# Kernel optimization log

Hardware: AMD Instinct MI355X
Metric: run time of the kernel (lower is better)

## Reference

```python
import jax, jax.numpy as jnp
import numpy as np

B, N, D = 16, 2048, 256  # batch (pairs*2), num_keypoints, descriptor_dim


def setup_inputs() -> dict:
    key = jax.random.key(0)
    k1, k2, k3, k4 = jax.random.split(key, 4)
    descriptors = jax.random.normal(k1, (B, N, D), dtype=jnp.float32)
    mask = jax.random.randint(k2, (B, N), 0, 2, dtype=jnp.int32)
    proj_w = jax.random.normal(k3, (D, D), dtype=jnp.float32) * 0.02
    proj_b = jnp.zeros((D,), dtype=jnp.float32)
    match_w = jax.random.normal(k4, (1, D), dtype=jnp.float32) * 0.02
    match_b = jnp.zeros((1,), dtype=jnp.float32)
    return {"descriptors": descriptors, "mask": mask, "proj_w": proj_w,
            "proj_b": proj_b, "match_w": match_w, "match_b": match_b}


def reference(descriptors, mask, proj_w, proj_b, match_w, match_b):
    batch, n, d = descriptors.shape
    pairs = batch // 2
    # final projection + temperature scaling
    m_desc = (descriptors @ proj_w.T + proj_b) / jnp.asarray(d, descriptors.dtype) ** 0.25
    m_desc = m_desc.reshape(pairs, 2, n, d)
    # similarity: [pairs, n0, n1]
    similarity = jnp.einsum('bnd,bmd->bnm', m_desc[:, 0], m_desc[:, 1])
    mask_p = mask.reshape(pairs, 2, n)
    pair_mask = mask_p[:, 0][:, :, None] * mask_p[:, 1][:, None, :]
    neg_min = jnp.finfo(similarity.dtype).min
    similarity = jnp.where(pair_mask == 0, neg_min, similarity)
    # matchability logits: [B, n, 1] -> split per pair
    matchability = (descriptors @ match_w.T + match_b).reshape(pairs, 2, n)
    m0 = matchability[:, 0]  # [pairs, n]
    m1 = matchability[:, 1]  # [pairs, n]
    certainties = jax.nn.log_sigmoid(m0)[:, :, None] + jax.nn.log_sigmoid(m1)[:, None, :]
    scores0 = jax.nn.log_softmax(similarity, axis=2)
    scores1 = jax.nn.log_softmax(similarity, axis=1)
    inner = scores0 + scores1 + certainties
    scores = jnp.zeros((pairs, n + 1, n + 1), dtype=similarity.dtype)
    scores = scores.at[:, :n, :n].set(inner)
    scores = scores.at[:, :-1, -1].set(jax.nn.log_sigmoid(-m0))
    scores = scores.at[:, -1, :-1].set(jax.nn.log_sigmoid(-m1))
    return scores
```

## Files before the change

### kernel.cpp

```cpp
#include <hip/hip_runtime.h>
#include <math.h>

typedef unsigned short u16;
typedef __attribute__((ext_vector_type(8))) short bf16x8;
typedef __attribute__((ext_vector_type(4))) float f32x4;

#define N 2048
#define D 256
#define PAIRS 8
#define NO 2049
#define NEGMIN  -3.40282347e38f
#define MASKVAL -3.0e38f
#define LDA 72
#define LDST 136

#define WS_LS0   0
#define WS_LS1   (1*PAIRS*N)
#define WS_LSN0  (2*PAIRS*N)
#define WS_LSN1  (3*PAIRS*N)
#define WS_CST   (6*PAIRS*N)
#define WS_RPM   (8*PAIRS*N)
#define WS_RPS   (WS_RPM + PAIRS*16*N)
#define WS_CPM   (WS_RPS + PAIRS*16*N)
#define WS_CPS   (WS_CPM + PAIRS*16*N)
#define WS_ROW   (WS_CPS + PAIRS*16*N)
#define WS_F_COUNT (WS_ROW + 4*PAIRS*N)

__device__ __forceinline__ float b2f(u16 u) {
    return __uint_as_float(((unsigned)u) << 16);
}
__device__ __forceinline__ u16 f2b(float f) {
    unsigned x = __float_as_uint(f);
    x += 0x7FFFu + ((x >> 16) & 1u);
    return (u16)(x >> 16);
}
__device__ __forceinline__ unsigned pk2(float a, float b) {
    return (unsigned)f2b(a) | ((unsigned)f2b(b) << 16);
}
__device__ __forceinline__ float logsig(float x) {
    return fminf(x, 0.f) - log1pf(expf(-fabsf(x)));
}
__device__ __forceinline__ void onmerge(float& m, float& s, float om, float os) {
    float nm = fmaxf(m, om);
    s = s * __expf(m - nm) + os * __expf(om - nm);
    m = nm;
}
__device__ __forceinline__ void gl_lds16(const u16* g, u16* l) {
    __builtin_amdgcn_global_load_lds(
        (const __attribute__((address_space(1))) unsigned*)(const void*)g,
        (__attribute__((address_space(3))) unsigned*)(void*)l, 16, 0, 0);
}

__global__ __launch_bounds__(256) void k_proj_mfma(const float* __restrict__ A,
                                                   const float* __restrict__ W,
                                                   const float* __restrict__ bias,
                                                   const float* __restrict__ mw,
                                                   const float* __restrict__ mb,
                                                   u16* __restrict__ mdesc,
                                                   float* __restrict__ wsf) {
    __shared__ union {
        struct { u16 A[128 * LDA]; u16 B[128 * LDA]; } t;
        u16 stage[128][LDST];
    } sh;
    int r0 = blockIdx.x * 128, c0 = blockIdx.y * 128;
    int tid = threadIdx.x;
    int w = tid >> 6, lane = tid & 63;
    int ln = lane & 15, q = lane >> 4;
    int wr0 = (w >> 1) * 64, wc0 = (w & 1) * 64;
    f32x4 zero = {0.f, 0.f, 0.f, 0.f};
    f32x4 acc[4][4];
    #pragma unroll
    for (int a = 0; a < 4; ++a)
        #pragma unroll
        for (int b = 0; b < 4; ++b) acc[a][b] = zero;
    float mdot[4] = {0.f, 0.f, 0.f, 0.f};
    int domatch = (blockIdx.y == 0);

    for (int kb = 0; kb < D; kb += 64) {
        __syncthreads();
        #pragma unroll
        for (int t = 0; t < 4; ++t) {
            int c = t * 256 + tid;
            int row = c >> 3, part = c & 7;
            const float* ap = A + (size_t)(r0 + row) * D + kb + part * 8;
            float4 f0 = *(const float4*)ap;
            float4 f1 = *(const float4*)(ap + 4);
            uint4 va;
            va.x = pk2(f0.x, f0.y); va.y = pk2(f0.z, f0.w);
            va.z = pk2(f1.x, f1.y); va.w = pk2(f1.z, f1.w);
            *(uint4*)&sh.t.A[row * LDA + part * 8] = va;
            if (domatch) {
                float4 w0 = *(const float4*)(mw + kb + part * 8);
                float4 w1 = *(const float4*)(mw + kb + part * 8 + 4);
                mdot[t] += f0.x*w0.x + f0.y*w0.y + f0.z*w0.z + f0.w*w0.w
                         + f1.x*w1.x + f1.y*w1.y + f1.z*w1.z + f1.w*w1.w;
            }
            const float* bp = W + (size_t)(c0 + row) * D + kb + part * 8;
            float4 g0 = *(const float4*)bp;
            float4 g1 = *(const float4*)(bp + 4);
            uint4 vb;
            vb.x = pk2(g0.x, g0.y); vb.y = pk2(g0.z, g0.w);
            vb.z = pk2(g1.x, g1.y); vb.w = pk2(g1.z, g1.w);
            *(uint4*)&sh.t.B[row * LDA + part * 8] = vb;
        }
        __syncthreads();
        #pragma unroll
        for (int kk = 0; kk < 64; kk += 32) {
            bf16x8 af[4], bf[4];
            #pragma unroll
            for (int ri = 0; ri < 4; ++ri)
                af[ri] = *(const bf16x8*)&sh.t.A[(wr0 + ri*16 + ln) * LDA + kk + q*8];
            #pragma unroll
            for (int ci = 0; ci < 4; ++ci)
                bf[ci] = *(const bf16x8*)&sh.t.B[(wc0 + ci*16 + ln) * LDA + kk + q*8];
            #pragma unroll
            for (int ri = 0; ri < 4; ++ri)
                #pragma unroll
                for (int ci = 0; ci < 4; ++ci)
                    acc[ri][ci] = __builtin_amdgcn_mfma_f32_16x16x32_bf16(af[ri], bf[ci], acc[ri][ci], 0, 0, 0);
        }
    }
    if (domatch) {
        #pragma unroll
        for (int t = 0; t < 4; ++t) {
            float s = mdot[t];
            s += __shfl_xor(s, 1, 64);
            s += __shfl_xor(s, 2, 64);
            s += __shfl_xor(s, 4, 64);
            if ((tid & 7) == 0) {
                int row_g = r0 + t * 32 + (tid >> 3);
                float m = s + mb[0];
                int b = row_g >> 11;
                int i = row_g & (N - 1);
                int pp = b >> 1, sid = b & 1;
                float ls = logsig(m), lsn = logsig(-m);
                if (sid == 0) { wsf[WS_LS0 + pp*N + i] = ls; wsf[WS_LSN0 + pp*N + i] = lsn; }
                else          { wsf[WS_LS1 + pp*N + i] = ls; wsf[WS_LSN1 + pp*N + i] = lsn; }
            }
        }
    }
    __syncthreads();
    #pragma unroll
    for (int ri = 0; ri < 4; ++ri) {
        #pragma unroll
        for (int reg = 0; reg < 4; ++reg) {
            int row_l = wr0 + ri*16 + q*4 + reg;
            #pragma unroll
            for (int ci = 0; ci < 4; ++ci) {
                int col = c0 + wc0 + ci*16 + ln;
                float v = (acc[ri][ci][reg] + bias[col]) * 0.25f;
                sh.stage[row_l][wc0 + ci*16 + ln] = f2b(v);
            }
        }
    }
    __syncthreads();
    {
        int row_l = tid >> 1, half = tid & 1;
        u16* dp = mdesc + (size_t)(r0 + row_l) * D + c0 + half * 64;
        const u16* lp = &sh.stage[row_l][half * 64];
        #pragma unroll
        for (int i = 0; i < 8; ++i)
            *(uint4*)(dp + i * 8) = *(const uint4*)(lp + i * 8);
    }
}

__global__ __launch_bounds__(256) void k_sim_mfma(const u16* __restrict__ mdesc,
                                                  const int* __restrict__ mask,
                                                  u16* __restrict__ sim,
                                                  float* __restrict__ wsf) {
    __shared__ union {
        u16 lds[4][128 * 64];
        u16 stage[128][LDST];
    } sh;
    __shared__ float rpm[128][2], rps[128][2];
    __shared__ float cpm[128][2], cps[128][2];
    int p = blockIdx.z;
    const u16* Am = mdesc + (size_t)(2*p) * N * D;
    const u16* Bm = mdesc + (size_t)(2*p + 1) * N * D;
    int r0 = blockIdx.x * 128, c0 = blockIdx.y * 128;
    int tid = threadIdx.x;
    int w = tid >> 6, lane = tid & 63;
    int ln = lane & 15, q = lane >> 4;
    int wr0 = (w >> 1) * 64, wc0 = (w & 1) * 64;
    int rsub = lane >> 3;
    int scol = (((lane & 7) ^ rsub) << 3);
    f32x4 zero = {0.f, 0.f, 0.f, 0.f};
    f32x4 acc[4][4];
    #pragma unroll
    for (int a = 0; a < 4; ++a)
        #pragma unroll
        for (int b = 0; b < 4; ++b) acc[a][b] = zero;

    #define STAGE(t_, bufi_) do {                                               \
        int kb_ = (t_) * 64;                                                    \
        u16* Ad_ = &sh.lds[(bufi_)*2][0];                                       \
        u16* Bd_ = &sh.lds[(bufi_)*2+1][0];                                     \
        _Pragma("unroll")                                                       \
        for (int j_ = 0; j_ < 4; ++j_) {                                        \
            int row_ = w * 32 + j_ * 8 + rsub;                                  \
            gl_lds16(Am + (size_t)(r0 + row_) * D + kb_ + scol,                 \
                     Ad_ + (w * 32 + j_ * 8) * 64);                             \
            gl_lds16(Bm + (size_t)(c0 + row_) * D + kb_ + scol,                 \
                     Bd_ + (w * 32 + j_ * 8) * 64);                             \
        }                                                                       \
    } while (0)

    STAGE(0, 0);
    __syncthreads();
    #pragma unroll
    for (int t = 0; t < 4; ++t) {
        int cur = t & 1;
        if (t < 3) STAGE(t + 1, cur ^ 1);
        const char* Abase = (const char*)&sh.lds[cur*2][0];
        const char* Bbase = (const char*)&sh.lds[cur*2+1][0];
        #pragma unroll
        for (int kk = 0; kk < 64; kk += 32) {
            bf16x8 af[4], bf[4];
            int cbase = kk * 2 + q * 16;
            int cswz = cbase ^ ((ln & 7) << 4);
            #pragma unroll
            for (int ri = 0; ri < 4; ++ri) {
                int row = wr0 + ri*16 + ln;
                af[ri] = *(const bf16x8*)(Abase + row * 128 + cswz);
            }
            #pragma unroll
            for (int ci = 0; ci < 4; ++ci) {
                int row = wc0 + ci*16 + ln;
                bf[ci] = *(const bf16x8*)(Bbase + row * 128 + cswz);
            }
            #pragma unroll
            for (int ri = 0; ri < 4; ++ri)
                #pragma unroll
                for (int ci = 0; ci < 4; ++ci)
                    acc[ri][ci] = __builtin_amdgcn_mfma_f32_16x16x32_bf16(af[ri], bf[ci], acc[ri][ci], 0, 0, 0);
        }
        __syncthreads();
    }
    #undef STAGE

    const int* m0 = mask + (size_t)(2*p) * N;
    const int* m1 = mask + (size_t)(2*p + 1) * N;
    int mcol[4];
    #pragma unroll
    for (int ci = 0; ci < 4; ++ci) mcol[ci] = m1[c0 + wc0 + ci*16 + ln];
    #pragma unroll
    for (int ri = 0; ri < 4; ++ri) {
        #pragma unroll
        for (int reg = 0; reg < 4; ++reg) {
            int row_l = wr0 + ri*16 + q*4 + reg;
            int mr = m0[r0 + row_l];
            #pragma unroll
            for (int ci = 0; ci < 4; ++ci) {
                float v = (mr && mcol[ci]) ? acc[ri][ci][reg] : MASKVAL;
                acc[ri][ci][reg] = v;
                sh.stage[row_l][wc0 + ci*16 + ln] = f2b(v);
            }
        }
    }
    #pragma unroll
    for (int ri = 0; ri < 4; ++ri) {
        #pragma unroll
        for (int reg = 0; reg < 4; ++reg) {
            float x0 = acc[ri][0][reg], x1 = acc[ri][1][reg];
            float x2 = acc[ri][2][reg], x3 = acc[ri][3][reg];
            float m = fmaxf(fmaxf(x0, x1), fmaxf(x2, x3));
            #pragma unroll
            for (int off = 1; off <= 8; off <<= 1)
                m = fmaxf(m, __shfl_xor(m, off, 64));
            float s = __expf(x0 - m) + __expf(x1 - m) + __expf(x2 - m) + __expf(x3 - m);
            #pragma unroll
            for (int off = 1; off <= 8; off <<= 1)
                s += __shfl_xor(s, off, 64);
            if (ln == 0) {
                int rl = wr0 + ri*16 + q*4 + reg;
                rpm[rl][w & 1] = m; rps[rl][w & 1] = s;
            }
        }
    }
    #pragma unroll
    for (int ci = 0; ci < 4; ++ci) {
        float m = acc[0][ci][0];
        #pragma unroll
        for (int ri = 0; ri < 4; ++ri)
            #pragma unroll
            for (int reg = 0; reg < 4; ++reg)
                if (!(ri == 0 && reg == 0)) m = fmaxf(m, acc[ri][ci][reg]);
        #pragma unroll
        for (int off = 16; off <= 32; off <<= 1)
            m = fmaxf(m, __shfl_xor(m, off, 64));
        float s = 0.f;
        #pragma unroll
        for (int ri = 0; ri < 4; ++ri)
            #pragma unroll
            for (int reg = 0; reg < 4; ++reg)
                s += __expf(acc[ri][ci][reg] - m);
        #pragma unroll
        for (int off = 16; off <= 32; off <<= 1)
            s += __shfl_xor(s, off, 64);
        if (q == 0) {
            int cl = wc0 + ci*16 + ln;
            cpm[cl][w >> 1] = m; cps[cl][w >> 1] = s;
        }
    }
    __syncthreads();
    {
        int row_l = tid >> 1, half = tid & 1;
        u16* sp = sim + ((size_t)p * N + r0 + row_l) * N + c0 + half * 64;
        const u16* lp = &sh.stage[row_l][half * 64];
        #pragma unroll
        for (int i = 0; i < 8; ++i)
            *(uint4*)(sp + i * 8) = *(const uint4*)(lp + i * 8);
    }
    if (tid < 128) {
        float m = rpm[tid][0], s = rps[tid][0];
        onmerge(m, s, rpm[tid][1], rps[tid][1]);
        size_t o = (size_t)(p * 16 + blockIdx.y) * N + r0 + tid;
        wsf[WS_RPM + o] = m; wsf[WS_RPS + o] = s;
    } else {
        int c = tid - 128;
        float m = cpm[c][0], s = cps[c][0];
        onmerge(m, s, cpm[c][1], cps[c][1]);
        size_t o = (size_t)(p * 16 + blockIdx.x) * N + c0 + c;
        wsf[WS_CPM + o] = m;
        wsf[WS_CPS + o] = s;
    }
}

__global__ __launch_bounds__(256) void k_red(float* __restrict__ wsf) {
    int i = blockIdx.x * 256 + threadIdx.x;
    int p = blockIdx.y;
    float m = wsf[WS_CPM + (size_t)(p*16) * N + i];
    float s = wsf[WS_CPS + (size_t)(p*16) * N + i];
    #pragma unroll
    for (int rb = 1; rb < 16; ++rb)
        onmerge(m, s, wsf[WS_CPM + (size_t)(p*16 + rb) * N + i],
                      wsf[WS_CPS + (size_t)(p*16 + rb) * N + i]);
    float2 cpack;
    cpack.x = -m - logf(s);
    cpack.y = wsf[WS_LS1 + p*N + i];
    *(float2*)&wsf[WS_CST + ((size_t)p * N + i) * 2] = cpack;
    float rm = wsf[WS_RPM + (size_t)(p*16) * N + i];
    float rs = wsf[WS_RPS + (size_t)(p*16) * N + i];
    #pragma unroll
    for (int rb = 1; rb < 16; ++rb)
        onmerge(rm, rs, wsf[WS_RPM + (size_t)(p*16 + rb) * N + i],
                        wsf[WS_RPS + (size_t)(p*16 + rb) * N + i]);
    float4 rpack;
    rpack.x = -rm - logf(rs);
    rpack.y = wsf[WS_LS0  + p*N + i];
    rpack.z = wsf[WS_LSN0 + p*N + i];
    rpack.w = 0.f;
    *(float4*)&wsf[WS_ROW + ((size_t)p * N + i) * 4] = rpack;
}

__global__ __launch_bounds__(256) void k_final(u16* __restrict__ out,
                                               const u16* __restrict__ sim,
                                               const float* __restrict__ wsf) {
    int strip = blockIdx.x;
    int p = blockIdx.y;
    int tid = threadIdx.x;
    unsigned* up = (unsigned*)out;
    if (strip == 256) {
        int head = p & 1;
        size_t B0 = ((size_t)p * NO + N) * NO;
        size_t U0 = (B0 + head) >> 1;
        const float* lsn1 = wsf + WS_LSN1 + p * N;
        #pragma unroll
        for (int k = 0; k < 4; ++k) {
            int kk = k * 256 + tid;
            int j0 = head + 2 * kk;
            float o0 = (j0 < N) ? lsn1[j0] : 0.f;
            float o1 = (j0 + 1 < N) ? lsn1[j0 + 1] : 0.f;
            up[U0 + kk] = pk2(o0, o1);
        }
        if (tid == 0) {
            if (head) out[B0] = f2b(lsn1[0]);
            else      out[B0 + N] = 0;
        }
        return;
    }
    __shared__ u16 stg[8][2052];
    int c8 = tid * 8;
    const float* cst = wsf + WS_CST + ((size_t)p * N + c8) * 2;
    float4 cs[4];
    #pragma unroll
    for (int k = 0; k < 4; ++k) cs[k] = *(const float4*)(cst + 4 * k);
    #pragma unroll
    for (int r = 0; r < 8; ++r) {
        int i = strip * 8 + r;
        int head = (p + i) & 1;
        float4 rsv = *(const float4*)&wsf[WS_ROW + ((size_t)p * N + i) * 4];
        float rc = rsv.x, l0 = rsv.y, ln0 = rsv.z;
        uint4 v = *(const uint4*)(sim + ((size_t)p * N + i) * N + c8);
        unsigned vv[4] = {v.x, v.y, v.z, v.w};
        float o[8];
        #pragma unroll
        for (int k = 0; k < 8; ++k) {
            float x = b2f((u16)(vv[k >> 1] >> ((k & 1) * 16)));
            float cA = ((const float*)&cs[0])[2 * k];
            float s1 = ((const float*)&cs[0])[2 * k + 1];
            float t = (x + rc) + (x + cA);
            o[k] = fmaxf(fmaxf(t, MASKVAL) + (l0 + s1), MASKVAL);
        }
        if (!head) {
            uint4 wv;
            wv.x = pk2(o[0], o[1]); wv.y = pk2(o[2], o[3]);
            wv.z = pk2(o[4], o[5]); wv.w = pk2(o[6], o[7]);
            *(uint4*)&stg[r][c8] = wv;
        } else {
            stg[r][c8 + 1] = f2b(o[0]);
            *(unsigned*)&stg[r][c8 + 2] = pk2(o[1], o[2]);
            *(unsigned*)&stg[r][c8 + 4] = pk2(o[3], o[4]);
            *(unsigned*)&stg[r][c8 + 6] = pk2(o[5], o[6]);
            stg[r][c8 + 8] = f2b(o[7]);
        }
        if (tid == 255) stg[r][2048 + head] = f2b(ln0);
    }
    __syncthreads();
    #pragma unroll
    for (int r = 0; r < 8; ++r) {
        int i = strip * 8 + r;
        int head = (p + i) & 1;
        size_t B0 = ((size_t)p * NO + i) * NO;
        size_t U0 = (B0 + head) >> 1;
        const unsigned* srow32 = (const unsigned*)&stg[r][0];
        #pragma unroll
        for (int k = 0; k < 4; ++k) {
            int kk = k * 256 + tid;
            up[U0 + kk] = srow32[kk + head];
        }
        if (tid == 0) {
            if (head) out[B0] = stg[r][1];
            else      out[B0 + N] = stg[r][2048];
        }
    }
}

extern "C" void kernel_launch(void* const* d_in, const int* in_sizes, int n_in,
                              void* d_out, int out_size, void* d_ws, size_t ws_size,
                              hipStream_t stream) {
    const float* desc    = (const float*)d_in[0];
    const int*   mask    = (const int*)d_in[1];
    const float* proj_w  = (const float*)d_in[2];
    const float* proj_b  = (const float*)d_in[3];
    const float* match_w = (const float*)d_in[4];
    const float* match_b = (const float*)d_in[5];
    u16*   out = (u16*)d_out;
    float* wsf = (float*)d_ws;
    u16*   mdesc = (u16*)((char*)d_ws + (size_t)WS_F_COUNT * sizeof(float));
    u16*   simw  = mdesc + (size_t)16 * N * D;

    k_proj_mfma<<<dim3(256, 2),    256, 0, stream>>>(desc, proj_w, proj_b, match_w, match_b, mdesc, wsf);
    k_sim_mfma <<<dim3(16, 16, 8), 256, 0, stream>>>(mdesc, mask, simw, wsf);
    k_red      <<<dim3(8, 8),      256, 0, stream>>>(wsf);
    k_final    <<<dim3(257, 8),    256, 0, stream>>>(out, simw, wsf);
}
```

Before: 257.6 us.

## Split fp32-to-bf16 conversion into a separate kernel and use direct LDS loads in projection

Adds a k_conv kernel that converts the descriptors and the projection weight to bf16 once and computes the matchability logsigmoids. The projection GEMM can then stream bf16 tiles straight into LDS with global_load_lds and a swizzled layout, instead of converting in registers every k-step. It also drops the double-buffered stage in the similarity kernel in favour of a single buffer, which may lower LDS use but loses the copy/compute overlap. The cost is an extra launch plus a write and re-read of a bf16 copy of the descriptors through the workspace.

```diff
diff --git a/kernel.cpp b/kernel.cpp
--- a/kernel.cpp
+++ b/kernel.cpp
@@ -11,7 +11,6 @@
 #define NO 2049
 #define NEGMIN  -3.40282347e38f
 #define MASKVAL -3.0e38f
-#define LDA 72
 #define LDST 136
 
 #define WS_LS0   0
@@ -51,15 +50,66 @@
         (__attribute__((address_space(3))) unsigned*)(void*)l, 16, 0, 0);
 }
 
-__global__ __launch_bounds__(256) void k_proj_mfma(const float* __restrict__ A,
-                                                   const float* __restrict__ W,
+__global__ __launch_bounds__(256) void k_conv(const float* __restrict__ desc,
+                                              const float* __restrict__ W,
+                                              const float* __restrict__ mw,
+                                              const float* __restrict__ mb,
+                                              u16* __restrict__ cdesc,
+                                              u16* __restrict__ wbf,
+                                              float* __restrict__ wsf) {
+    int tid = threadIdx.x;
+    int blk = blockIdx.x;
+    if (blk == 256) {
+        const float* src = W + (size_t)tid * 256;
+        u16* dst = wbf + (size_t)tid * 256;
+        #pragma unroll
+        for (int i = 0; i < 256; i += 8) {
+            float4 f0 = *(const float4*)(src + i);
+            float4 f1 = *(const float4*)(src + i + 4);
+            uint4 v;
+            v.x = pk2(f0.x, f0.y); v.y = pk2(f0.z, f0.w);
+            v.z = pk2(f1.x, f1.y); v.w = pk2(f1.z, f1.w);
+            *(uint4*)(dst + i) = v;
+        }
+        return;
+    }
+    int row_l = tid >> 1, half = tid & 1;
+    int row_g = blk * 128 + row_l;
+    const float* src = desc + (size_t)row_g * D + half * 128;
+    u16* dst = cdesc + (size_t)row_g * D + half * 128;
+    const float* mwp = mw + half * 128;
+    float dot = 0.f;
+    #pragma unroll
+    for (int i = 0; i < 128; i += 8) {
+        float4 f0 = *(const float4*)(src + i);
+        float4 f1 = *(const float4*)(src + i + 4);
+        uint4 v;
+        v.x = pk2(f0.x, f0.y); v.y = pk2(f0.z, f0.w);
+        v.z = pk2(f1.x, f1.y); v.w = pk2(f1.z, f1.w);
+        *(uint4*)(dst + i) = v;
+        float4 w0 = *(const float4*)(mwp + i);
+        float4 w1 = *(const float4*)(mwp + i + 4);
+        dot += f0.x*w0.x + f0.y*w0.y + f0.z*w0.z + f0.w*w0.w
+             + f1.x*w1.x + f1.y*w1.y + f1.z*w1.z + f1.w*w1.w;
+    }
+    dot += __shfl_xor(dot, 1, 64);
+    if (half == 0) {
+        float m = dot + mb[0];
+        int b = row_g >> 11;
+        int i = row_g & (N - 1);
+        int pp = b >> 1, sid = b & 1;
+        float ls = logsig(m), lsn = logsig(-m);
+        if (sid == 0) { wsf[WS_LS0 + pp*N + i] = ls; wsf[WS_LSN0 + pp*N + i] = lsn; }
+        else          { wsf[WS_LS1 + pp*N + i] = ls; wsf[WS_LSN1 + pp*N + i] = lsn; }
+    }
+}
+
+__global__ __launch_bounds__(256) void k_proj_mfma(const u16* __restrict__ cdesc,
+                                                   const u16* __restrict__ wbf,
                                                    const float* __restrict__ bias,
-                                                   const float* __restrict__ mw,
-                                                   const float* __restrict__ mb,
-                                                   u16* __restrict__ mdesc,
-                                                   float* __restrict__ wsf) {
+                                                   u16* __restrict__ mdesc) {
     __shared__ union {
-        struct { u16 A[128 * LDA]; u16 B[128 * LDA]; } t;
+        struct { u16 A[128 * 64]; u16 B[128 * 64]; } t;
         u16 stage[128][LDST];
     } sh;
     int r0 = blockIdx.x * 128, c0 = blockIdx.y * 128;
@@ -67,79 +117,51 @@
     int w = tid >> 6, lane = tid & 63;
     int ln = lane & 15, q = lane >> 4;
     int wr0 = (w >> 1) * 64, wc0 = (w & 1) * 64;
+    int rsub = lane >> 3;
+    int scol = (((lane & 7) ^ rsub) << 3);
+    const u16* Am = cdesc + (size_t)r0 * D;
+    const u16* Bm = wbf + (size_t)c0 * D;
     f32x4 zero = {0.f, 0.f, 0.f, 0.f};
     f32x4 acc[4][4];
     #pragma unroll
     for (int a = 0; a < 4; ++a)
         #pragma unroll
         for (int b = 0; b < 4; ++b) acc[a][b] = zero;
-    float mdot[4] = {0.f, 0.f, 0.f, 0.f};
-    int domatch = (blockIdx.y == 0);
 
     for (int kb = 0; kb < D; kb += 64) {
-        __syncthreads();
-        #pragma unroll
-        for (int t = 0; t < 4; ++t) {
-            int c = t * 256 + tid;
-            int row = c >> 3, part = c & 7;
-            const float* ap = A + (size_t)(r0 + row) * D + kb + part * 8;
-            float4 f0 = *(const float4*)ap;
-            float4 f1 = *(const float4*)(ap + 4);
-            uint4 va;
-            va.x = pk2(f0.x, f0.y); va.y = pk2(f0.z, f0.w);
-            va.z = pk2(f1.x, f1.y); va.w = pk2(f1.z, f1.w);
-            *(uint4*)&sh.t.A[row * LDA + part * 8] = va;
-            if (domatch) {
-                float4 w0 = *(const float4*)(mw + kb + part * 8);
-                float4 w1 = *(const float4*)(mw + kb + part * 8 + 4);
-                mdot[t] += f0.x*w0.x + f0.y*w0.y + f0.z*w0.z + f0.w*w0.w
-                         + f1.x*w1.x + f1.y*w1.y + f1.z*w1.z + f1.w*w1.w;
-            }
-            const float* bp = W + (size_t)(c0 + row) * D + kb + part * 8;
-            float4 g0 = *(const float4*)bp;
-            float4 g1 = *(const float4*)(bp + 4);
-            uint4 vb;
-            vb.x = pk2(g0.x, g0.y); vb.y = pk2(g0.z, g0.w);
-            vb.z = pk2(g1.x, g1.y); vb.w = pk2(g1.z, g1.w);
-            *(uint4*)&sh.t.B[row * LDA + part * 8] = vb;
+        #pragma unroll
+        for (int j = 0; j < 4; ++j) {
+            int row = w * 32 + j * 8 + rsub;
+            gl_lds16(Am + (size_t)row * D + kb + scol, &sh.t.A[(w * 32 + j * 8) * 64]);
+            gl_lds16(Bm + (size_t)row * D + kb + scol, &sh.t.B[(w * 32 + j * 8) * 64]);
         }
         __syncthreads();
         #pragma unroll
         for (int kk = 0; kk < 64; kk += 32) {
             bf16x8 af[4], bf[4];
-            #pragma unroll
-            for (int ri = 0; ri < 4; ++ri)
-                af[ri] = *(const bf16x8*)&sh.t.A[(wr0 + ri*16 + ln) * LDA + kk + q*8];
-            #pragma unroll
-            for (int ci = 0; ci < 4; ++ci)
-                bf[ci] = *(const bf16x8*)&sh.t.B[(wc0 + ci*16 + ln) * LDA + kk + q*8];
+            int cbase = kk * 2 + q * 16;
+            int cswz = cbase ^ ((ln & 7) << 4);
+            #pragma unroll
+            for (int ri = 0; ri < 4; ++ri) {
+                int row = wr0 + ri*16 + ln;
+                af[ri] = *(const bf16x8*)((const char*)sh.t.A + row * 128 + cswz);
+            }
+            #pragma unroll
+            for (int ci = 0; ci < 4; ++ci) {
+                int row = wc0 + ci*16 + ln;
+                bf[ci] = *(const bf16x8*)((const char*)sh.t.B + row * 128 + cswz);
+            }
             #pragma unroll
             for (int ri = 0; ri < 4; ++ri)
                 #pragma unroll
                 for (int ci = 0; ci < 4; ++ci)
                     acc[ri][ci] = __builtin_amdgcn_mfma_f32_16x16x32_bf16(af[ri], bf[ci], acc[ri][ci], 0, 0, 0);
         }
-    }
-    if (domatch) {
-        #pragma unroll
-        for (int t = 0; t < 4; ++t) {
-            float s = mdot[t];
-            s += __shfl_xor(s, 1, 64);
-            s += __shfl_xor(s, 2, 64);
-            s += __shfl_xor(s, 4, 64);
-            if ((tid & 7) == 0) {
-                int row_g = r0 + t * 32 + (tid >> 3);
-                float m = s + mb[0];
-                int b = row_g >> 11;
-                int i = row_g & (N - 1);
-                int pp = b >> 1, sid = b & 1;
-                float ls = logsig(m), lsn = logsig(-m);
-                if (sid == 0) { wsf[WS_LS0 + pp*N + i] = ls; wsf[WS_LSN0 + pp*N + i] = lsn; }
-                else          { wsf[WS_LS1 + pp*N + i] = ls; wsf[WS_LSN1 + pp*N + i] = lsn; }
-            }
-        }
-    }
-    __syncthreads();
+        __syncthreads();
+    }
+    float bs[4];
+    #pragma unroll
+    for (int ci = 0; ci < 4; ++ci) bs[ci] = bias[c0 + wc0 + ci*16 + ln];
     #pragma unroll
     for (int ri = 0; ri < 4; ++ri) {
         #pragma unroll
@@ -147,8 +169,7 @@
             int row_l = wr0 + ri*16 + q*4 + reg;
             #pragma unroll
             for (int ci = 0; ci < 4; ++ci) {
-                int col = c0 + wc0 + ci*16 + ln;
-                float v = (acc[ri][ci][reg] + bias[col]) * 0.25f;
+                float v = (acc[ri][ci][reg] + bs[ci]) * 0.25f;
                 sh.stage[row_l][wc0 + ci*16 + ln] = f2b(v);
             }
         }
@@ -169,7 +190,7 @@
                                                   u16* __restrict__ sim,
                                                   float* __restrict__ wsf) {
     __shared__ union {
-        u16 lds[4][128 * 64];
+        struct { u16 A[128 * 64]; u16 B[128 * 64]; } t;
         u16 stage[128][LDST];
     } sh;
     __shared__ float rpm[128][2], rps[128][2];
@@ -191,28 +212,14 @@
         #pragma unroll
         for (int b = 0; b < 4; ++b) acc[a][b] = zero;
 
-    #define STAGE(t_, bufi_) do {                                               \
-        int kb_ = (t_) * 64;                                                    \
-        u16* Ad_ = &sh.lds[(bufi_)*2][0];                                       \
-        u16* Bd_ = &sh.lds[(bufi_)*2+1][0];                                     \
-        _Pragma("unroll")                                                       \
-        for (int j_ = 0; j_ < 4; ++j_) {                                        \
-            int row_ = w * 32 + j_ * 8 + rsub;                                  \
-            gl_lds16(Am + (size_t)(r0 + row_) * D + kb_ + scol,                 \
-                     Ad_ + (w * 32 + j_ * 8) * 64);                             \
-            gl_lds16(Bm + (size_t)(c0 + row_) * D + kb_ + scol,                 \
-                     Bd_ + (w * 32 + j_ * 8) * 64);                             \
-        }                                                                       \
-    } while (0)
-
-    STAGE(0, 0);
-    __syncthreads();
-    #pragma unroll
-    for (int t = 0; t < 4; ++t) {
-        int cur = t & 1;
-        if (t < 3) STAGE(t + 1, cur ^ 1);
-        const char* Abase = (const char*)&sh.lds[cur*2][0];
-        const char* Bbase = (const char*)&sh.lds[cur*2+1][0];
+    for (int kb = 0; kb < D; kb += 64) {
+        #pragma unroll
+        for (int j = 0; j < 4; ++j) {
+            int row = w * 32 + j * 8 + rsub;
+            gl_lds16(Am + (size_t)(r0 + row) * D + kb + scol, &sh.t.A[(w * 32 + j * 8) * 64]);
+            gl_lds16(Bm + (size_t)(c0 + row) * D + kb + scol, &sh.t.B[(w * 32 + j * 8) * 64]);
+        }
+        __syncthreads();
         #pragma unroll
         for (int kk = 0; kk < 64; kk += 32) {
             bf16x8 af[4], bf[4];
@@ -221,12 +228,12 @@
             #pragma unroll
             for (int ri = 0; ri < 4; ++ri) {
                 int row = wr0 + ri*16 + ln;
-                af[ri] = *(const bf16x8*)(Abase + row * 128 + cswz);
+                af[ri] = *(const bf16x8*)((const char*)sh.t.A + row * 128 + cswz);
             }
             #pragma unroll
             for (int ci = 0; ci < 4; ++ci) {
                 int row = wc0 + ci*16 + ln;
-                bf[ci] = *(const bf16x8*)(Bbase + row * 128 + cswz);
+                bf[ci] = *(const bf16x8*)((const char*)sh.t.B + row * 128 + cswz);
             }
             #pragma unroll
             for (int ri = 0; ri < 4; ++ri)
@@ -236,8 +243,6 @@
         }
         __syncthreads();
     }
-    #undef STAGE
-
     const int* m0 = mask + (size_t)(2*p) * N;
     const int* m1 = mask + (size_t)(2*p + 1) * N;
     int mcol[4];
@@ -449,8 +454,11 @@
     float* wsf = (float*)d_ws;
     u16*   mdesc = (u16*)((char*)d_ws + (size_t)WS_F_COUNT * sizeof(float));
     u16*   simw  = mdesc + (size_t)16 * N * D;
-
-    k_proj_mfma<<<dim3(256, 2),    256, 0, stream>>>(desc, proj_w, proj_b, match_w, match_b, mdesc, wsf);
+    u16*   cdesc = simw + (size_t)PAIRS * N * N;
+    u16*   wbf   = cdesc + (size_t)16 * N * D;
+
+    k_conv     <<<257,             256, 0, stream>>>(desc, proj_w, match_w, match_b, cdesc, wbf, wsf);
+    k_proj_mfma<<<dim3(256, 2),    256, 0, stream>>>(cdesc, wbf, proj_b, mdesc);
     k_sim_mfma <<<dim3(16, 16, 8), 256, 0, stream>>>(mdesc, mask, simw, wsf);
     k_red      <<<dim3(8, 8),      256, 0, stream>>>(wsf);
     k_final    <<<dim3(257, 8),    256, 0, stream>>>(out, simw, wsf);
```

Measured after the change: 281.2 us. 9.2% more time.
